# Performance work log

Hardware: AMD Instinct MI355X
Metric: run time of the kernel (lower is better)

## Reference

```python
import jax, jax.numpy as jnp
import numpy as np

EPS = 1e-6  # flax.linen.LayerNorm default

def layer_norm(x, scale, bias):
    mean = jnp.mean(x, axis=-1, keepdims=True)
    var = jnp.mean(jnp.square(x - mean), axis=-1, keepdims=True)
    return (x - mean) * jax.lax.rsqrt(var + EPS) * scale + bias

def setup_inputs() -> dict:
    key = jax.random.key(0)
    ks = jax.random.split(key, 4)
    B, P, D, H = 2, 2048, 768, 12
    hd = D // H
    x = jax.random.normal(ks[0], (B, P, D), dtype=jnp.float32)
    W_qkv = jax.random.normal(ks[1], (D, 3 * D), dtype=jnp.float32) * (D ** -0.5)
    W_out = jax.random.normal(ks[2], (D, D), dtype=jnp.float32) * (D ** -0.5)
    b_out = jnp.zeros((D,), dtype=jnp.float32)
    return {
        "x": x,
        "W_qkv": W_qkv,
        "q_scale": jnp.ones((hd,), jnp.float32),
        "q_bias": jnp.zeros((hd,), jnp.float32),
        "k_scale": jnp.ones((hd,), jnp.float32),
        "k_bias": jnp.zeros((hd,), jnp.float32),
        "o_scale": jnp.ones((D,), jnp.float32),
        "o_bias": jnp.zeros((D,), jnp.float32),
        "W_out": W_out,
        "b_out": b_out,
    }

def reference(x, W_qkv, q_scale, q_bias, k_scale, k_bias, o_scale, o_bias, W_out, b_out):
    B, P, D = x.shape
    H = 12
    hd = D // H
    scale = hd ** -0.5
    # fused QKV projection, no bias
    qkv = (x @ W_qkv).reshape(B, P, 3, H, hd).transpose(2, 0, 3, 1, 4)  # [3,B,H,P,hd]
    q, k, v = qkv[0], qkv[1], qkv[2]
    # per-head QK LayerNorm over head_dim
    q = layer_norm(q, q_scale, q_bias) * scale
    k = layer_norm(k, k_scale, k_bias)
    attn = jnp.einsum("bhqd,bhkd->bhqk", q, k)
    attn = jax.nn.softmax(attn, axis=-1)
    out = jnp.einsum("bhqk,bhkd->bhqd", attn, v)  # [B,H,P,hd]
    out = jnp.swapaxes(out, 1, 2).reshape(B, P, D)
    out = layer_norm(out, o_scale, o_bias)
    return out @ W_out + b_out
```

## Files before the change

### kernel.cpp

```cpp
#include <hip/hip_runtime.h>
#include <hip/hip_bf16.h>

#define B_  2
#define P_  2048
#define D_  768
#define H_  12
#define HD_ 64
#define M_  (B_ * P_)
#define N1_ (3 * D_)

typedef __attribute__((ext_vector_type(8))) short short8;
typedef __attribute__((ext_vector_type(4))) float f32x4;
typedef __attribute__((ext_vector_type(16))) float f32x16;
typedef __attribute__((ext_vector_type(4))) unsigned u32x4;
typedef unsigned short ushort;

__device__ __forceinline__ ushort f2bf(float f) {
    unsigned u = __float_as_uint(f);
    u += 0x7fffu + ((u >> 16) & 1u);
    return (ushort)(u >> 16);
}

__device__ __forceinline__ unsigned cvtpk(float a, float b) {
    unsigned r;
    asm("v_cvt_pk_bf16_f32 %0, %1, %2" : "=v"(r) : "v"(a), "v"(b));
    return r;
}

__device__ __forceinline__ int swap23(int s) {
    return (s & ~12) | ((s & 4) << 1) | ((s & 8) >> 1);
}

#define QSC_ (0.125f * 1.44269504088896340736f)

__global__ __launch_bounds__(512) void gemm_qkv_mfma(
        const float* __restrict__ x, const float* __restrict__ w,
        const float* __restrict__ qs, const float* __restrict__ qb,
        const float* __restrict__ ks, const float* __restrict__ kb,
        ushort* __restrict__ qkv) {
    __shared__ __align__(16) ushort As[128][40];
    __shared__ __align__(16) ushort Bs[128][40];

    const int tid  = threadIdx.x;
    const int lane = tid & 63;
    const int wv   = tid >> 6;
    const int quad = lane >> 4;
    const int col  = lane & 15;
    const int wr   = (wv >> 1) * 32;
    const int wc   = (wv & 1) * 64;
    const int rowBase = blockIdx.y * 128;
    const int colBase = blockIdx.x * 128;

    const int am0 = tid >> 3, ac4 = tid & 7;
    const int nB  = tid & 127, kq = tid >> 7;

    float4 apre[2];
    float  bpre[8];
    auto load_tile = [&](int kt) {
        const int k0 = kt * 32;
        apre[0] = *(const float4*)(x + (size_t)(rowBase + am0) * D_ + k0 + ac4 * 4);
        apre[1] = *(const float4*)(x + (size_t)(rowBase + am0 + 64) * D_ + k0 + ac4 * 4);
#pragma unroll
        for (int j = 0; j < 8; j++)
            bpre[j] = w[(size_t)(k0 + kq * 8 + j) * N1_ + colBase + nB];
    };

    f32x4 acc[2][4];
#pragma unroll
    for (int i = 0; i < 2; i++)
#pragma unroll
        for (int j = 0; j < 4; j++) acc[i][j] = (f32x4){0.f, 0.f, 0.f, 0.f};

    load_tile(0);
    const int NT = D_ / 32;
    for (int kt = 0; kt < NT; kt++) {
        __syncthreads();
        {
            uint2 a0 = {cvtpk(apre[0].x, apre[0].y), cvtpk(apre[0].z, apre[0].w)};
            uint2 a1 = {cvtpk(apre[1].x, apre[1].y), cvtpk(apre[1].z, apre[1].w)};
            *(uint2*)&As[am0][ac4 * 4]      = a0;
            *(uint2*)&As[am0 + 64][ac4 * 4] = a1;
            u32x4 bb;
#pragma unroll
            for (int j = 0; j < 4; j++) bb[j] = cvtpk(bpre[2 * j], bpre[2 * j + 1]);
            *(u32x4*)&Bs[nB][kq * 8] = bb;
        }
        __syncthreads();
        if (kt + 1 < NT) load_tile(kt + 1);

        short8 af[2], bf[4];
#pragma unroll
        for (int mt = 0; mt < 2; mt++) af[mt] = *(const short8*)&As[wr + mt * 16 + col][quad * 8];
#pragma unroll
        for (int nt = 0; nt < 4; nt++) bf[nt] = *(const short8*)&Bs[wc + nt * 16 + col][quad * 8];
#pragma unroll
        for (int mt = 0; mt < 2; mt++)
#pragma unroll
            for (int nt = 0; nt < 4; nt++)
                acc[mt][nt] = __builtin_amdgcn_mfma_f32_16x16x32_bf16(af[mt], bf[nt], acc[mt][nt], 0, 0, 0);
    }

    const int comp = colBase / D_;
    const int rem  = colBase + wc - comp * D_;
    const int h    = rem >> 6;
    float sc4[4] = {0, 0, 0, 0}, bi4[4] = {0, 0, 0, 0};
    if (comp == 0) {
#pragma unroll
        for (int nt = 0; nt < 4; nt++) { sc4[nt] = qs[nt * 16 + col]; bi4[nt] = qb[nt * 16 + col]; }
    } else if (comp == 1) {
#pragma unroll
        for (int nt = 0; nt < 4; nt++) { sc4[nt] = ks[nt * 16 + col]; bi4[nt] = kb[nt * 16 + col]; }
    }

#pragma unroll
    for (int mt = 0; mt < 2; mt++) {
#pragma unroll
        for (int r = 0; r < 4; r++) {
            int m  = rowBase + wr + mt * 16 + quad * 4 + r;
            int bb = m >> 11;
            int p  = m & 2047;
            float v0 = acc[mt][0][r], v1 = acc[mt][1][r], v2 = acc[mt][2][r], v3 = acc[mt][3][r];
            if (comp < 2) {
                float s = v0 + v1 + v2 + v3;
#pragma unroll
                for (int off = 1; off < 16; off <<= 1) s += __shfl_xor(s, off, 64);
                float mean = s * (1.0f / 64.0f);
                float d0 = v0 - mean, d1 = v1 - mean, d2 = v2 - mean, d3 = v3 - mean;
                float sq = d0 * d0 + d1 * d1 + d2 * d2 + d3 * d3;
#pragma unroll
                for (int off = 1; off < 16; off <<= 1) sq += __shfl_xor(sq, off, 64);
                float inv = rsqrtf(sq * (1.0f / 64.0f) + 1e-6f);
                v0 = d0 * inv * sc4[0] + bi4[0];
                v1 = d1 * inv * sc4[1] + bi4[1];
                v2 = d2 * inv * sc4[2] + bi4[2];
                v3 = d3 * inv * sc4[3] + bi4[3];
                if (comp == 0) { v0 *= QSC_; v1 *= QSC_; v2 *= QSC_; v3 *= QSC_; }
            }
            size_t base = ((((size_t)comp * B_ + bb) * H_ + h) * P_ + p) * HD_;
            qkv[base +  0 + col] = f2bf(v0);
            qkv[base + 16 + col] = f2bf(v1);
            qkv[base + 32 + col] = f2bf(v2);
            qkv[base + 48 + col] = f2bf(v3);
        }
    }
}

__global__ __launch_bounds__(256) void attn_split(const ushort* __restrict__ qkv,
                                                  float* __restrict__ o0, float* __restrict__ o1,
                                                  float* __restrict__ o2, float* __restrict__ o3,
                                                  float* __restrict__ l0, float* __restrict__ l1,
                                                  float* __restrict__ l2, float* __restrict__ l3) {
    const int p0  = blockIdx.x * 128;
    const int bh  = blockIdx.y;
    const int s   = blockIdx.z;
    const int nsp = gridDim.z;
    const int b   = bh / H_, h = bh % H_;
    float* opart = (s == 0) ? o0 : (s == 1) ? o1 : (s == 2) ? o2 : o3;
    float* lpart = (s == 0) ? l0 : (s == 1) ? l1 : (s == 2) ? l2 : l3;
    const int tid  = threadIdx.x;
    const int lane = tid & 63;
    const int wv   = tid >> 6;
    const int half = lane >> 5;
    const int n32  = lane & 31;

    __shared__ __align__(16) ushort KVs[2][64][72];
    ushort (&Ks)[64][72] = KVs[0];
    ushort (&Vs)[64][72] = KVs[1];

    const size_t hs  = (size_t)P_ * HD_;
    const int    kv0 = s * (P_ / nsp);
    const ushort* qg = qkv + ((size_t)(0 * B_ + b) * H_ + h) * hs + (size_t)(p0 + wv * 32) * HD_;
    const ushort* kg = qkv + ((size_t)(1 * B_ + b) * H_ + h) * hs + (size_t)kv0 * HD_;
    const ushort* vg = qkv + ((size_t)(2 * B_ + b) * H_ + h) * hs + (size_t)kv0 * HD_;

    short8 aq[4];
#pragma unroll
    for (int ks2 = 0; ks2 < 4; ks2++)
        aq[ks2] = *(const short8*)(qg + (size_t)n32 * HD_ + ks2 * 16 + half * 8);

    float lsum = 0.f;
    f32x16 oaccT[2];
#pragma unroll
    for (int nt = 0; nt < 2; nt++)
#pragma unroll
        for (int r = 0; r < 16; r++) oaccT[nt][r] = 0.f;

    const int kr = tid >> 3, kc8 = tid & 7;
    const int krs = swap23(kr);
    const int vd = tid & 63,  vkh = tid >> 6;

    uint4  kpre[2];
    ushort vpre[16];
    auto load_tile = [&](int kt) {
        const ushort* kg_t = kg + (size_t)kt * 64 * HD_;
        const ushort* vg_t = vg + (size_t)kt * 64 * HD_;
        kpre[0] = *(const uint4*)(kg_t + (size_t)kr * HD_ + kc8 * 8);
        kpre[1] = *(const uint4*)(kg_t + (size_t)(kr + 32) * HD_ + kc8 * 8);
#pragma unroll
        for (int j = 0; j < 16; j++)
            vpre[j] = vg_t[(size_t)(vkh * 16 + j) * HD_ + vd];
    };

    load_tile(0);
    const int NT = (P_ / 64) / nsp;
    for (int kt = 0; kt < NT; kt++) {
        __syncthreads();
        *(uint4*)&Ks[krs][kc8 * 8]      = kpre[0];
        *(uint4*)&Ks[krs + 32][kc8 * 8] = kpre[1];
        *(short8*)&Vs[vd][vkh * 16]     = *(short8*)&vpre[0];
        *(short8*)&Vs[vd][vkh * 16 + 8] = *(short8*)&vpre[8];
        __syncthreads();
        if (kt + 1 < NT) load_tile(kt + 1);

        u32x4 pw[2][2];
#pragma unroll
        for (int nt = 0; nt < 2; nt++) {
            f32x16 sc;
#pragma unroll
            for (int r = 0; r < 16; r++) sc[r] = 0.f;
#pragma unroll
            for (int ks2 = 0; ks2 < 4; ks2++) {
                short8 kb2 = *(const short8*)&Ks[nt * 32 + n32][ks2 * 16 + half * 8];
                sc = __builtin_amdgcn_mfma_f32_32x32x16_bf16(kb2, aq[ks2], sc, 0, 0, 0);
            }
            float p[16];
#pragma unroll
            for (int r = 0; r < 16; r++) {
                p[r] = __builtin_amdgcn_exp2f(fminf(sc[r], 86.5f));
                lsum += p[r];
            }
#pragma unroll
            for (int kp2 = 0; kp2 < 2; kp2++)
#pragma unroll
                for (int i = 0; i < 4; i++)
                    pw[nt][kp2][i] = cvtpk(p[kp2 * 8 + 2 * i], p[kp2 * 8 + 2 * i + 1]);
        }

#pragma unroll
        for (int kstep = 0; kstep < 4; kstep++) {
            short8 pb = __builtin_bit_cast(short8, pw[kstep >> 1][kstep & 1]);
#pragma unroll
            for (int ntd = 0; ntd < 2; ntd++) {
                short8 av = *(const short8*)&Vs[ntd * 32 + n32][kstep * 16 + half * 8];
                oaccT[ntd] = __builtin_amdgcn_mfma_f32_32x32x16_bf16(av, pb, oaccT[ntd], 0, 0, 0);
            }
        }
    }

    lsum += __shfl_xor(lsum, 32, 64);
    if (lane < 32)
        lpart[(size_t)bh * P_ + p0 + wv * 32 + lane] = lsum;

    __syncthreads();
    float* scr = (float*)&KVs[0][0][0] + wv * 1152;
#pragma unroll
    for (int ntd = 0; ntd < 2; ntd++) {
#pragma unroll
        for (int r = 0; r < 16; r++)
            scr[n32 * 36 + (r & 3) + 8 * (r >> 2) + 4 * half] = oaccT[ntd][r];
#pragma unroll
        for (int i = 0; i < 4; i++) {
            int ql = i * 8 + (lane >> 3);
            int c4 = lane & 7;
            float4 v = *(const float4*)&scr[ql * 36 + c4 * 4];
            *(float4*)(opart + ((size_t)bh * P_ + p0 + wv * 32 + ql) * HD_ + ntd * 32 + c4 * 4) = v;
        }
    }
}

__global__ __launch_bounds__(256) void ln_o(const float* __restrict__ o0,
                                            const float* __restrict__ o1,
                                            const float* __restrict__ o2,
                                            const float* __restrict__ o3,
                                            const float* __restrict__ l0,
                                            const float* __restrict__ l1,
                                            const float* __restrict__ l2,
                                            const float* __restrict__ l3,
                                            const int ns,
                                            ushort* __restrict__ lnb,
                                            const float* __restrict__ osc,
                                            const float* __restrict__ ob) {
    __shared__ float red[4];
    __shared__ float red2[4];
    const int row = blockIdx.x;
    const int b   = row >> 11;
    const int p   = row & (P_ - 1);
    const int tid = threadIdx.x;

    auto src = [&](int d) {
        int h = d >> 6;
        size_t lr  = (size_t)(b * H_ + h) * P_ + p;
        size_t idx = lr * HD_ + (d & 63);
        float num = o0[idx] + o1[idx];
        float den = l0[lr] + l1[lr];
        if (ns == 4) { num += o2[idx] + o3[idx]; den += l2[lr] + l3[lr]; }
        return num / den;
    };
    float v0 = src(tid);
    float v1 = src(tid + 256);
    float v2 = src(tid + 512);
    float s = v0 + v1 + v2;
#pragma unroll
    for (int o = 32; o > 0; o >>= 1) s += __shfl_xor(s, o, 64);
    if ((tid & 63) == 0) red[tid >> 6] = s;
    __syncthreads();
    float mean = (red[0] + red[1] + red[2] + red[3]) * (1.0f / 768.0f);
    float d0 = v0 - mean, d1 = v1 - mean, d2 = v2 - mean;
    float sq = d0 * d0 + d1 * d1 + d2 * d2;
#pragma unroll
    for (int o = 32; o > 0; o >>= 1) sq += __shfl_xor(sq, o, 64);
    if ((tid & 63) == 0) red2[tid >> 6] = sq;
    __syncthreads();
    float var = (red2[0] + red2[1] + red2[2] + red2[3]) * (1.0f / 768.0f);
    float inv = rsqrtf(var + 1e-6f);
    const size_t base = (size_t)row * D_;
    lnb[base + tid]       = f2bf(d0 * inv * osc[tid]       + ob[tid]);
    lnb[base + tid + 256] = f2bf(d1 * inv * osc[tid + 256] + ob[tid + 256]);
    lnb[base + tid + 512] = f2bf(d2 * inv * osc[tid + 512] + ob[tid + 512]);
}

__global__ __launch_bounds__(256) void gemm_out_mfma(
        const ushort* __restrict__ a, const float* __restrict__ w,
        const float* __restrict__ bias, float* __restrict__ out) {
    __shared__ __align__(16) ushort As[64][40];
    __shared__ __align__(16) ushort Bs[64][40];

    const int tid  = threadIdx.x;
    const int lane = tid & 63;
    const int wv   = tid >> 6;
    const int quad = lane >> 4;
    const int col  = lane & 15;
    const int wr   = (wv >> 1) * 32;
    const int wc   = (wv & 1) * 32;
    const int rowBase = blockIdx.y * 64;
    const int colBase = blockIdx.x * 64;

    const int am  = tid >> 2, ac8 = tid & 3;
    const int nB  = tid & 63, kq = tid >> 6;

    uint4 apre;
    float bpre[8];
    auto load_tile = [&](int kt) {
        const int k0 = kt * 32;
        apre = *(const uint4*)(a + (size_t)(rowBase + am) * D_ + k0 + ac8 * 8);
#pragma unroll
        for (int j = 0; j < 8; j++)
            bpre[j] = w[(size_t)(k0 + kq * 8 + j) * D_ + colBase + nB];
    };

    f32x4 acc[2][2];
#pragma unroll
    for (int i = 0; i < 2; i++)
#pragma unroll
        for (int j = 0; j < 2; j++) acc[i][j] = (f32x4){0.f, 0.f, 0.f, 0.f};

    load_tile(0);
    const int NT = D_ / 32;
    for (int kt = 0; kt < NT; kt++) {
        __syncthreads();
        *(uint4*)&As[am][ac8 * 8] = apre;
        {
            u32x4 bb;
#pragma unroll
            for (int j = 0; j < 4; j++) bb[j] = cvtpk(bpre[2 * j], bpre[2 * j + 1]);
            *(u32x4*)&Bs[nB][kq * 8] = bb;
        }
        __syncthreads();
        if (kt + 1 < NT) load_tile(kt + 1);

        short8 af[2], bf[2];
#pragma unroll
        for (int mt = 0; mt < 2; mt++) af[mt] = *(const short8*)&As[wr + mt * 16 + col][quad * 8];
#pragma unroll
        for (int nt = 0; nt < 2; nt++) bf[nt] = *(const short8*)&Bs[wc + nt * 16 + col][quad * 8];
#pragma unroll
        for (int mt = 0; mt < 2; mt++)
#pragma unroll
            for (int nt = 0; nt < 2; nt++)
                acc[mt][nt] = __builtin_amdgcn_mfma_f32_16x16x32_bf16(af[mt], bf[nt], acc[mt][nt], 0, 0, 0);
    }

    float b2[2];
#pragma unroll
    for (int nt = 0; nt < 2; nt++) b2[nt] = bias[colBase + wc + nt * 16 + col];
#pragma unroll
    for (int mt = 0; mt < 2; mt++) {
#pragma unroll
        for (int r = 0; r < 4; r++) {
            int m = rowBase + wr + mt * 16 + quad * 4 + r;
            float* dst = out + (size_t)m * D_ + colBase + wc;
#pragma unroll
            for (int nt = 0; nt < 2; nt++)
                dst[nt * 16 + col] = acc[mt][nt][r] + b2[nt];
        }
    }
}

extern "C" void kernel_launch(void* const* d_in, const int* in_sizes, int n_in,
                              void* d_out, int out_size, void* d_ws, size_t ws_size,
                              hipStream_t stream) {
    const float* x    = (const float*)d_in[0];
    const float* Wqkv = (const float*)d_in[1];
    const float* qs   = (const float*)d_in[2];
    const float* qb   = (const float*)d_in[3];
    const float* ks   = (const float*)d_in[4];
    const float* kb   = (const float*)d_in[5];
    const float* osc  = (const float*)d_in[6];
    const float* ob   = (const float*)d_in[7];
    const float* Wout = (const float*)d_in[8];
    const float* bout = (const float*)d_in[9];
    float* out = (float*)d_out;

    ushort* qkv = (ushort*)d_ws;
    const size_t qkvE = (size_t)3 * B_ * H_ * P_ * HD_;
    const size_t oE   = (size_t)B_ * H_ * P_ * HD_;
    const size_t lE   = (size_t)B_ * H_ * P_;
    float* base = (float*)(qkv + qkvE);
    const size_t need4 = qkvE * sizeof(ushort) + (3 * oE + 4 * lE) * sizeof(float);
    const int nsp = (ws_size >= need4) ? 4 : 2;
    float* op[4];
    float* lbase;
    if (nsp == 4) {
        op[0] = base; op[1] = base + oE; op[2] = base + 2 * oE; op[3] = out;
        lbase = base + 3 * oE;
    } else {
        op[0] = base; op[1] = out; op[2] = base; op[3] = base;
        lbase = base + oE;
    }
    float* lp[4] = {lbase, lbase + lE, lbase + 2 * lE, lbase + 3 * lE};
    ushort* ln_buf = qkv;

    gemm_qkv_mfma<<<dim3(N1_ / 128, M_ / 128), 512, 0, stream>>>(x, Wqkv, qs, qb, ks, kb, qkv);
    attn_split<<<dim3(P_ / 128, B_ * H_, nsp), 256, 0, stream>>>(
        qkv, op[0], op[1], op[2], op[3], lp[0], lp[1], lp[2], lp[3]);
    ln_o<<<dim3(M_), 256, 0, stream>>>(
        op[0], op[1], op[2], op[3], lp[0], lp[1], lp[2], lp[3], nsp, ln_buf, osc, ob);
    gemm_out_mfma<<<dim3(D_ / 64, M_ / 64), 256, 0, stream>>>(ln_buf, Wout, bout, out);
}
```

Before: 201.5 us.

## Double-buffer K/V tiles in LDS and interleave PV MFMAs per score tile

The attention split kernel now keeps two K/V tile buffers in shared memory. The next tile is staged into the idle buffer after compute, so each iteration needs one barrier instead of two. The P·V MFMAs are issued right after each 32-key score tile is exponentiated, rather than after both tiles, which shortens register live ranges. The exp2 clamp is dropped, and so is the barrier before the epilogue reuses shared memory as scratch. That second removal is only safe because the final iteration reads the other buffer when the tile count is even, and dropping the clamp relies on the QK LayerNorm keeping scores bounded.

```diff
diff --git a/kernel.cpp b/kernel.cpp
--- a/kernel.cpp
+++ b/kernel.cpp
@@ -163,9 +163,7 @@
     const int half = lane >> 5;
     const int n32  = lane & 31;
 
-    __shared__ __align__(16) ushort KVs[2][64][72];
-    ushort (&Ks)[64][72] = KVs[0];
-    ushort (&Vs)[64][72] = KVs[1];
+    __shared__ __align__(16) ushort KVs[2][2][64][72];
 
     const size_t hs  = (size_t)P_ * HD_;
     const int    kv0 = s * (P_ / nsp);
@@ -200,19 +198,26 @@
         for (int j = 0; j < 16; j++)
             vpre[j] = vg_t[(size_t)(vkh * 16 + j) * HD_ + vd];
     };
+    auto stage = [&](int buf) {
+        *(uint4*)&KVs[buf][0][krs][kc8 * 8]      = kpre[0];
+        *(uint4*)&KVs[buf][0][krs + 32][kc8 * 8] = kpre[1];
+        *(short8*)&KVs[buf][1][vd][vkh * 16]     = *(short8*)&vpre[0];
+        *(short8*)&KVs[buf][1][vd][vkh * 16 + 8] = *(short8*)&vpre[8];
+    };
 
     load_tile(0);
+    stage(0);
+    __syncthreads();
+
     const int NT = (P_ / 64) / nsp;
+    int cur = 0;
     for (int kt = 0; kt < NT; kt++) {
-        __syncthreads();
-        *(uint4*)&Ks[krs][kc8 * 8]      = kpre[0];
-        *(uint4*)&Ks[krs + 32][kc8 * 8] = kpre[1];
-        *(short8*)&Vs[vd][vkh * 16]     = *(short8*)&vpre[0];
-        *(short8*)&Vs[vd][vkh * 16 + 8] = *(short8*)&vpre[8];
-        __syncthreads();
-        if (kt + 1 < NT) load_tile(kt + 1);
-
-        u32x4 pw[2][2];
+        const bool more = (kt + 1 < NT);
+        if (more) load_tile(kt + 1);
+
+        ushort (*Ks)[72] = KVs[cur][0];
+        ushort (*Vs)[72] = KVs[cur][1];
+
 #pragma unroll
         for (int nt = 0; nt < 2; nt++) {
             f32x16 sc;
@@ -226,24 +231,29 @@
             float p[16];
 #pragma unroll
             for (int r = 0; r < 16; r++) {
-                p[r] = __builtin_amdgcn_exp2f(fminf(sc[r], 86.5f));
+                p[r] = __builtin_amdgcn_exp2f(sc[r]);
                 lsum += p[r];
             }
-#pragma unroll
-            for (int kp2 = 0; kp2 < 2; kp2++)
-#pragma unroll
-                for (int i = 0; i < 4; i++)
-                    pw[nt][kp2][i] = cvtpk(p[kp2 * 8 + 2 * i], p[kp2 * 8 + 2 * i + 1]);
-        }
-
-#pragma unroll
-        for (int kstep = 0; kstep < 4; kstep++) {
-            short8 pb = __builtin_bit_cast(short8, pw[kstep >> 1][kstep & 1]);
-#pragma unroll
-            for (int ntd = 0; ntd < 2; ntd++) {
-                short8 av = *(const short8*)&Vs[ntd * 32 + n32][kstep * 16 + half * 8];
-                oaccT[ntd] = __builtin_amdgcn_mfma_f32_32x32x16_bf16(av, pb, oaccT[ntd], 0, 0, 0);
+            unsigned w[8];
+#pragma unroll
+            for (int i = 0; i < 8; i++) w[i] = cvtpk(p[2 * i], p[2 * i + 1]);
+#pragma unroll
+            for (int kp2 = 0; kp2 < 2; kp2++) {
+                u32x4 t = {w[kp2 * 4 + 0], w[kp2 * 4 + 1], w[kp2 * 4 + 2], w[kp2 * 4 + 3]};
+                short8 pb = __builtin_bit_cast(short8, t);
+                const int kstep = nt * 2 + kp2;
+#pragma unroll
+                for (int ntd = 0; ntd < 2; ntd++) {
+                    short8 av = *(const short8*)&Vs[ntd * 32 + n32][kstep * 16 + half * 8];
+                    oaccT[ntd] = __builtin_amdgcn_mfma_f32_32x32x16_bf16(av, pb, oaccT[ntd], 0, 0, 0);
+                }
             }
+        }
+
+        if (more) {
+            stage(cur ^ 1);
+            __syncthreads();
+            cur ^= 1;
         }
     }
 
@@ -251,8 +261,7 @@
     if (lane < 32)
         lpart[(size_t)bh * P_ + p0 + wv * 32 + lane] = lsum;
 
-    __syncthreads();
-    float* scr = (float*)&KVs[0][0][0] + wv * 1152;
+    float* scr = (float*)&KVs[0][0][0][0] + wv * 1152;
 #pragma unroll
     for (int ntd = 0; ntd < 2; ntd++) {
 #pragma unroll
```

New measurement: 199.3 us. About the same (-1.1%).
